# Kernel optimization log

Measured on AMD Instinct MI355X. Metric: run time of the kernel, lower is better.

## Reference

```python
import jax, jax.numpy as jnp
import numpy as np

HIDDEN = 2048
HEADS = 16
HEAD_DIM = HIDDEN // HEADS


def setup_inputs() -> dict:
    key = jax.random.key(0)
    ks = jax.random.split(key, 9)
    s = 0.02
    return {
        "hidden_state": jax.random.normal(ks[0], (2, 2048, HIDDEN), dtype=jnp.float32),
        "Wq": jax.random.normal(ks[1], (HIDDEN, HIDDEN), dtype=jnp.float32) * s,
        "bq": jnp.zeros((HIDDEN,), dtype=jnp.float32),
        "Wk": jax.random.normal(ks[2], (HIDDEN, HIDDEN), dtype=jnp.float32) * s,
        "bk": jnp.zeros((HIDDEN,), dtype=jnp.float32),
        "Wv": jax.random.normal(ks[3], (HIDDEN, HIDDEN), dtype=jnp.float32) * s,
        "bv": jnp.zeros((HIDDEN,), dtype=jnp.float32),
        "Wo": jax.random.normal(ks[4], (HIDDEN, HIDDEN), dtype=jnp.float32) * s,
        "bo": jnp.zeros((HIDDEN,), dtype=jnp.float32),
    }


def _split_head(x):
    b, s, _ = x.shape
    return x.reshape(b, s, HEADS, HEAD_DIM).transpose(0, 2, 1, 3)  # [B,H,S,D]


def reference(hidden_state, Wq, bq, Wk, bk, Wv, bv, Wo, bo):
    scale = 1.0 / (HEAD_DIM ** 0.5)
    # nn.Linear: x @ W.T + b
    q = _split_head(hidden_state @ Wq.T + bq)
    k = _split_head(hidden_state @ Wk.T + bk)
    v = _split_head(hidden_state @ Wv.T + bv)
    scores = jnp.einsum("bhqd,bhkd->bhqk", q, k) * scale  # [B,H,S,S]
    probs = jax.nn.softmax(scores, axis=-1)
    # dropout treated as identity (eval mode)
    out = jnp.einsum("bhqk,bhkd->bhqd", probs, v)  # [B,H,S,D]
    b, h, s, d = out.shape
    out = out.transpose(0, 2, 1, 3).reshape(b, s, h * d)
    return out @ Wo.T + bo
```

## Files before the change

kernel.cpp:

```cpp
#include <hip/hip_runtime.h>
#include <hip/hip_bf16.h>


typedef __attribute__((ext_vector_type(8))) short bf16x8;
typedef __attribute__((ext_vector_type(4))) float f32x4;
typedef unsigned short ushort_t;

#define MFMA_16x16x32(a, b, c) __builtin_amdgcn_mfma_f32_16x16x32_bf16((a), (b), (c), 0, 0, 0)

__device__ __forceinline__ ushort_t f2bf(float f) {
  unsigned int u = __builtin_bit_cast(unsigned int, f);
  u += 0x7fffu + ((u >> 16) & 1u);
  return (ushort_t)(u >> 16);
}

__device__ __forceinline__ void gload_lds16(const void* g, void* lds) {
  __builtin_amdgcn_global_load_lds(
      (const __attribute__((address_space(1))) unsigned int*)g,
      (__attribute__((address_space(3))) unsigned int*)(unsigned int)(unsigned long long)lds,
      16, 0, 0);
}

__global__ __launch_bounds__(256) void f2bf_kernel(const float* __restrict__ in,
                                                   ushort_t* __restrict__ out, int n4) {
  int i = blockIdx.x * blockDim.x + threadIdx.x;
  const int stride = gridDim.x * blockDim.x;
  for (; i < n4; i += stride) {
    const float4 v = ((const float4*)in)[i];
    ushort4 o;
    o.x = f2bf(v.x); o.y = f2bf(v.y); o.z = f2bf(v.z); o.w = f2bf(v.w);
    ((ushort4*)out)[i] = o;
  }
}

template <int SWAPV>
__global__ __launch_bounds__(512) void qkv_gemm(
    const ushort_t* __restrict__ A,
    const ushort_t* __restrict__ W,
    const float* __restrict__ bq, const float* __restrict__ bk,
    const float* __restrict__ bv,
    ushort_t* __restrict__ Qs, ushort_t* __restrict__ Ks,
    ushort_t* __restrict__ Vts, int nbx, int bcol0) {
  constexpr int K = 2048, NT = K / 32;
  extern __shared__ char sm[];
  const int tid = threadIdx.x;
  const int wave = tid >> 6, lane = tid & 63;
  const int g = lane >> 4, l15 = lane & 15;
  const int wr = wave >> 2, wc = wave & 3;

  const int bid = blockIdx.x;
  const int chunk = (nbx * 16) >> 3;
  const int sw = (bid & 7) * chunk + (bid >> 3);
  const int bx = sw % nbx, by = sw / nbx;
  const int brow = by * 256, bcol = bcol0 + bx * 256;

  const ushort_t* srcA[2];
  const ushort_t* srcB[2];
#pragma unroll
  for (int j = 0; j < 2; ++j) {
    const int p = (wave * 2 + j) * 64 + lane;
    const int row = p >> 2;
    const int col = (p & 3) ^ ((row >> 1) & 3);
    srcA[j] = A + (size_t)(brow + row) * K + col * 8;
    srcB[j] = W + (size_t)(bcol + row) * K + col * 8;
  }

  const int fph = (l15 >> 1) & 3;
  const int aOff = (wr * 128 + l15) * 64 + ((g ^ fph) << 4);
  const int bOff = (wc * 64 + l15) * 64 + ((g ^ fph) << 4) + 16384;

  char* p0 = sm;
  char* p1 = sm + 32768;
  char* p2 = sm + 65536;

#define STAGE_A(P, t)                                                        \
  {                                                                          \
    gload_lds16(srcA[0] + (t) * 32, (P) + (wave * 2 + 0) * 1024);            \
    gload_lds16(srcA[1] + (t) * 32, (P) + (wave * 2 + 1) * 1024);            \
  }
#define STAGE_B(P, t)                                                        \
  {                                                                          \
    gload_lds16(srcB[0] + (t) * 32, (P) + 16384 + (wave * 2 + 0) * 1024);    \
    gload_lds16(srcB[1] + (t) * 32, (P) + 16384 + (wave * 2 + 1) * 1024);    \
  }

  const f32x4 fzero = {0.f, 0.f, 0.f, 0.f};
  f32x4 acc[8][4];
#pragma unroll
  for (int i = 0; i < 8; ++i)
#pragma unroll
    for (int j = 0; j < 4; ++j) acc[i][j] = fzero;

  STAGE_A(p0, 0); STAGE_B(p0, 0);
  STAGE_A(p1, 1); STAGE_B(p1, 1);
  asm volatile("s_waitcnt vmcnt(4)" ::: "memory");
  __builtin_amdgcn_sched_barrier(0);
  __builtin_amdgcn_s_barrier();
  __builtin_amdgcn_sched_barrier(0);

  for (int kt = 0; kt < NT; ++kt) {
    const bool doStage = (kt < NT - 2);
    if (doStage) STAGE_A(p2, kt + 2);
    bf16x8 bfr[4], afr[4];
#pragma unroll
    for (int j = 0; j < 4; ++j) bfr[j] = *(const bf16x8*)(p0 + bOff + j * 1024);
#pragma unroll
    for (int i = 0; i < 4; ++i) afr[i] = *(const bf16x8*)(p0 + aOff + i * 1024);
    __builtin_amdgcn_s_setprio(1);
#pragma unroll
    for (int i = 0; i < 4; ++i)
#pragma unroll
      for (int j = 0; j < 4; ++j)
        acc[i][j] = SWAPV ? MFMA_16x16x32(bfr[j], afr[i], acc[i][j])
                          : MFMA_16x16x32(afr[i], bfr[j], acc[i][j]);
    __builtin_amdgcn_s_setprio(0);
    if (doStage) STAGE_B(p2, kt + 2);
#pragma unroll
    for (int i = 0; i < 4; ++i) afr[i] = *(const bf16x8*)(p0 + aOff + (4 + i) * 1024);
    __builtin_amdgcn_s_setprio(1);
#pragma unroll
    for (int i = 0; i < 4; ++i)
#pragma unroll
      for (int j = 0; j < 4; ++j)
        acc[4 + i][j] = SWAPV ? MFMA_16x16x32(bfr[j], afr[i], acc[4 + i][j])
                              : MFMA_16x16x32(afr[i], bfr[j], acc[4 + i][j]);
    __builtin_amdgcn_s_setprio(0);
    if (doStage) {
      asm volatile("s_waitcnt vmcnt(4) lgkmcnt(0)" ::: "memory");
    } else {
      asm volatile("s_waitcnt vmcnt(0) lgkmcnt(0)" ::: "memory");
    }
    __builtin_amdgcn_sched_barrier(0);
    __builtin_amdgcn_s_barrier();
    __builtin_amdgcn_sched_barrier(0);
    char* t = p0; p0 = p1; p1 = p2; p2 = t;
  }
#undef STAGE_A
#undef STAGE_B

  if (!SWAPV) {
    const int seg = bcol >> 11;
    const float* bias = (seg == 0) ? bq : bk;
    ushort_t* out = (seg == 0) ? Qs : Ks;
#pragma unroll
    for (int j = 0; j < 4; ++j) {
      const int n = (bcol + wc * 64 + j * 16 + l15) & 2047;
      const float bb = bias[n];
      const int h = n >> 7, d = n & 127;
#pragma unroll
      for (int i = 0; i < 8; ++i) {
#pragma unroll
        for (int r = 0; r < 4; ++r) {
          const int grow = brow + wr * 128 + i * 16 + g * 4 + r;
          const int b_ = grow >> 11, s_ = grow & 2047;
          out[(((size_t)b_ * 16 + h) * 2048 + s_) * 128 + d] =
              f2bf(acc[i][j][r] + bb);
        }
      }
    }
  } else {
#pragma unroll
    for (int j = 0; j < 4; ++j) {
#pragma unroll
      for (int r = 0; r < 4; ++r) {
        const int n = (bcol + wc * 64 + j * 16 + g * 4 + r) & 2047;
        const float bb = bv[n];
        const int h = n >> 7, d = n & 127;
#pragma unroll
        for (int i = 0; i < 8; ++i) {
          const int m = brow + wr * 128 + i * 16 + l15;
          const int b_ = m >> 11, s_ = m & 2047;
          Vts[(((size_t)b_ * 16 + h) * 128 + d) * 2048 + s_] =
              f2bf(acc[i][j][r] + bb);
        }
      }
    }
  }
}

__global__ __launch_bounds__(256) void gemm_bt_kernel(const ushort_t* __restrict__ A,
                                                      const ushort_t* __restrict__ B,
                                                      const float* __restrict__ bias,
                                                      float* __restrict__ Cout,
                                                      int M, int N, int K) {
  __shared__ __align__(16) char smem[16384];
  char* sA = smem;
  char* sB = smem + 8192;
  const int tid = threadIdx.x;
  const int wave = tid >> 6;
  const int lane = tid & 63;
  const int wr = wave >> 1, wc = wave & 1;
  const int brow = blockIdx.y * 128;
  const int bcol = blockIdx.x * 128;

  const f32x4 fzero = {0.f, 0.f, 0.f, 0.f};
  f32x4 acc[4][4];
#pragma unroll
  for (int i = 0; i < 4; ++i)
#pragma unroll
    for (int j = 0; j < 4; ++j) acc[i][j] = fzero;

  const int srow = lane >> 2;
  const int koff = (lane & 3) * 8;

  for (int kt = 0; kt < K; kt += 32) {
#pragma unroll
    for (int c = 0; c < 2; ++c) {
      const int ch = wave + c * 4;
      gload_lds16(A + (size_t)(brow + ch * 16 + srow) * K + kt + koff, sA + ch * 1024);
      gload_lds16(B + (size_t)(bcol + ch * 16 + srow) * K + kt + koff, sB + ch * 1024);
    }
    __syncthreads();
    bf16x8 af[4], bfr[4];
#pragma unroll
    for (int i = 0; i < 4; ++i)
      af[i] = *(const bf16x8*)(sA + (wr * 64 + i * 16 + (lane & 15)) * 64 + (lane >> 4) * 16);
#pragma unroll
    for (int j = 0; j < 4; ++j)
      bfr[j] = *(const bf16x8*)(sB + (wc * 64 + j * 16 + (lane & 15)) * 64 + (lane >> 4) * 16);
#pragma unroll
    for (int i = 0; i < 4; ++i)
#pragma unroll
      for (int j = 0; j < 4; ++j) acc[i][j] = MFMA_16x16x32(af[i], bfr[j], acc[i][j]);
    __syncthreads();
  }

#pragma unroll
  for (int i = 0; i < 4; ++i)
#pragma unroll
    for (int j = 0; j < 4; ++j)
#pragma unroll
      for (int r = 0; r < 4; ++r) {
        const int row = brow + wr * 64 + i * 16 + (lane >> 4) * 4 + r;
        const int col = bcol + wc * 64 + j * 16 + (lane & 15);
        Cout[(size_t)row * N + col] = acc[i][j][r] + bias[col];
      }
}

__global__ __launch_bounds__(256) void attn_kernel(const ushort_t* __restrict__ Q,
                                                   const ushort_t* __restrict__ K,
                                                   const ushort_t* __restrict__ Vt,
                                                   ushort_t* __restrict__ O) {
  constexpr int S = 2048, D = 128, H = 16;
  __shared__ __align__(16) char smem[16384 + 16384 + 9216];
  char* sK = smem;
  char* sVt = smem + 16384;
  char* sP = smem + 32768;

  const int tid = threadIdx.x;
  const int wave = tid >> 6;
  const int lane = tid & 63;
  const int g = lane >> 4;
  const int l15 = lane & 15;
  const int qt = blockIdx.x & 31;
  const int bh = blockIdx.x >> 5;
  const int b = bh >> 4, h = bh & 15;

  const ushort_t* Qb = Q + (size_t)bh * S * D;
  const char* Kb = (const char*)(K + (size_t)bh * S * D);
  const char* Vtb = (const char*)(Vt + (size_t)bh * D * S);
  const int q0 = qt * 64 + wave * 16;

  bf16x8 aq[4];
  {
    const ushort_t* qrow = Qb + (size_t)(q0 + l15) * D + g * 8;
#pragma unroll
    for (int kk = 0; kk < 4; ++kk) aq[kk] = *(const bf16x8*)(qrow + kk * 32);
  }

  const char* kg[4];
  const char* vg[4];
#pragma unroll
  for (int i = 0; i < 4; ++i) {
    const int po = (wave * 4 + i) * 1024 + lane * 16;
    const int lk = po ^ (((po >> 8) & 7) << 4);
    kg[i] = Kb + (size_t)(lk >> 8) * 256 + (lk & 255);
    const int lv = po ^ (((po >> 7) & 7) << 4);
    vg[i] = Vtb + (size_t)(lv >> 7) * 4096 + (lv & 127);
  }

  const f32x4 fzero = {0.f, 0.f, 0.f, 0.f};
  f32x4 o[8];
#pragma unroll
  for (int nt = 0; nt < 8; ++nt) o[nt] = fzero;
  float row_m[4] = {-1e30f, -1e30f, -1e30f, -1e30f};
  float row_l[4] = {0.f, 0.f, 0.f, 0.f};

  bf16x8 ones;
#pragma unroll
  for (int i = 0; i < 8; ++i) ones[i] = (short)0x3F80;

  char* sPw = sP + wave * 2304;
  const float SC = 0.12751746f;
  const float THR = 90.0f;

  for (int kv0 = 0; kv0 < S; kv0 += 64) {
    __syncthreads();
#pragma unroll
    for (int i = 0; i < 4; ++i)
      gload_lds16(kg[i] + (size_t)kv0 * 256, sK + (wave * 4 + i) * 1024);
#pragma unroll
    for (int i = 0; i < 4; ++i)
      gload_lds16(vg[i] + (size_t)kv0 * 2, sVt + (wave * 4 + i) * 1024);
    __syncthreads();

    f32x4 sfrag[4];
#pragma unroll
    for (int nt = 0; nt < 4; ++nt) {
      sfrag[nt] = fzero;
#pragma unroll
      for (int kk = 0; kk < 4; ++kk) {
        const int row = nt * 16 + l15;
        const int la = row * 256 + kk * 64 + g * 16;
        const bf16x8 bk = *(const bf16x8*)(sK + (la ^ ((row & 7) << 4)));
        sfrag[nt] = MFMA_16x16x32(aq[kk], bk, sfrag[nt]);
      }
    }

#pragma unroll
    for (int r = 0; r < 4; ++r) {
      const float s0 = sfrag[0][r];
      const float s1 = sfrag[1][r];
      const float s2 = sfrag[2][r];
      const float s3 = sfrag[3][r];
      const float lm = fmaxf(fmaxf(s0, s1), fmaxf(s2, s3));
      if (!__all(lm - row_m[r] <= THR)) {
        float mx = lm;
        mx = fmaxf(mx, __shfl_xor(mx, 1));
        mx = fmaxf(mx, __shfl_xor(mx, 2));
        mx = fmaxf(mx, __shfl_xor(mx, 4));
        mx = fmaxf(mx, __shfl_xor(mx, 8));
        const float nm = fmaxf(row_m[r], mx);
        const float corr = exp2f((row_m[r] - nm) * SC);
        row_l[r] *= corr;
#pragma unroll
        for (int nt = 0; nt < 8; ++nt) o[nt][r] *= corr;
        row_m[r] = nm;
      }
      const float nm = row_m[r];
      const float p0 = exp2f((s0 - nm) * SC);
      const float p1 = exp2f((s1 - nm) * SC);
      const float p2 = exp2f((s2 - nm) * SC);
      const float p3 = exp2f((s3 - nm) * SC);
      unsigned int pk01, pk23;
      asm("v_cvt_pk_bf16_f32 %0, %1, %2" : "=v"(pk01) : "v"(p0), "v"(p1));
      asm("v_cvt_pk_bf16_f32 %0, %1, %2" : "=v"(pk23) : "v"(p2), "v"(p3));
      ushort_t* pr = (ushort_t*)(sPw + (g * 4 + r) * 144);
      pr[l15] = (ushort_t)(pk01 & 0xffffu);
      pr[16 + l15] = (ushort_t)(pk01 >> 16);
      pr[32 + l15] = (ushort_t)(pk23 & 0xffffu);
      pr[48 + l15] = (ushort_t)(pk23 >> 16);
    }

    const bf16x8 pa0 = *(const bf16x8*)(sPw + l15 * 144 + g * 16);
    const bf16x8 pa1 = *(const bf16x8*)(sPw + l15 * 144 + 64 + g * 16);
    f32x4 lfrag = fzero;
    lfrag = MFMA_16x16x32(pa0, ones, lfrag);
    lfrag = MFMA_16x16x32(pa1, ones, lfrag);
#pragma unroll
    for (int nt = 0; nt < 8; ++nt) {
      const int d = nt * 16 + l15;
      const int la0 = d * 128 + g * 16;
      const bf16x8 bv0 = *(const bf16x8*)(sVt + (la0 ^ ((d & 7) << 4)));
      o[nt] = MFMA_16x16x32(pa0, bv0, o[nt]);
      const bf16x8 bv1 = *(const bf16x8*)(sVt + ((la0 + 64) ^ ((d & 7) << 4)));
      o[nt] = MFMA_16x16x32(pa1, bv1, o[nt]);
    }
#pragma unroll
    for (int r = 0; r < 4; ++r) row_l[r] += lfrag[r];
  }

#pragma unroll
  for (int r = 0; r < 4; ++r) {
    const float inv = 1.0f / row_l[r];
    const int srow = q0 + g * 4 + r;
    ushort_t* orow = O + ((size_t)b * S + srow) * (H * D) + h * D;
#pragma unroll
    for (int nt = 0; nt < 8; ++nt) orow[nt * 16 + l15] = f2bf(o[nt][r] * inv);
  }
}

extern "C" void kernel_launch(void* const* d_in, const int* in_sizes, int n_in,
                              void* d_out, int out_size, void* d_ws, size_t ws_size,
                              hipStream_t stream) {
  const float* hidden = (const float*)d_in[0];
  const float* Wq = (const float*)d_in[1];
  const float* bq = (const float*)d_in[2];
  const float* Wk = (const float*)d_in[3];
  const float* bk = (const float*)d_in[4];
  const float* Wv = (const float*)d_in[5];
  const float* bv = (const float*)d_in[6];
  const float* Wo = (const float*)d_in[7];
  const float* bo = (const float*)d_in[8];

  constexpr int M = 4096, N = 2048, Kd = 2048;
  char* ws = (char*)d_ws;
  ushort_t* hb   = (ushort_t*)(ws);
  ushort_t* wqkv = (ushort_t*)(ws + (16u << 20));
  ushort_t* wob  = (ushort_t*)(ws + (40u << 20));
  ushort_t* Qs   = (ushort_t*)(ws + (48u << 20));
  ushort_t* Ks   = Qs + (size_t)M * N;
  ushort_t* Vts  = Ks + (size_t)M * N;
  ushort_t* AO   = Vts + (size_t)M * N;

  f2bf_kernel<<<2048, 256, 0, stream>>>(hidden, hb, M * Kd / 4);
  f2bf_kernel<<<1024, 256, 0, stream>>>(Wq, wqkv, N * Kd / 4);
  f2bf_kernel<<<1024, 256, 0, stream>>>(Wk, wqkv + (size_t)N * Kd, N * Kd / 4);
  f2bf_kernel<<<1024, 256, 0, stream>>>(Wv, wqkv + 2 * (size_t)N * Kd, N * Kd / 4);
  f2bf_kernel<<<1024, 256, 0, stream>>>(Wo, wob, N * Kd / 4);

  qkv_gemm<0><<<256, 512, 98304, stream>>>(hb, wqkv, bq, bk, bv, Qs, Ks, Vts, 16, 0);
  qkv_gemm<1><<<128, 512, 98304, stream>>>(hb, wqkv, bq, bk, bv, Qs, Ks, Vts, 8, 4096);
  attn_kernel<<<1024, 256, 0, stream>>>(Qs, Ks, Vts, AO);
  dim3 gg(N / 128, M / 128);
  gemm_bt_kernel<<<gg, 256, 0, stream>>>(AO, wob, bo, (float*)d_out, M, N, Kd);
}
```

Baseline: 489.5 us.

## Replace output projection with triple-buffered 256x256 tiled GEMM and merge weight casts

Replaces the simple 128x128 output-projection GEMM with a 512-thread kernel using 256x256 tiles. It triple-buffers LDS loads with swizzled layout, interleaves staging with MFMA, and raises wave priority during MFMA. The four weight bf16 conversion launches are merged into one kernel, and attention is split into two launches over halves of the batch-heads. The larger tiles launch only 128 blocks, which may underfill the GPU.

```diff
diff --git a/kernel.cpp b/kernel.cpp
--- a/kernel.cpp
+++ b/kernel.cpp
@@ -26,6 +26,24 @@
   int i = blockIdx.x * blockDim.x + threadIdx.x;
   const int stride = gridDim.x * blockDim.x;
   for (; i < n4; i += stride) {
+    const float4 v = ((const float4*)in)[i];
+    ushort4 o;
+    o.x = f2bf(v.x); o.y = f2bf(v.y); o.z = f2bf(v.z); o.w = f2bf(v.w);
+    ((ushort4*)out)[i] = o;
+  }
+}
+
+__global__ __launch_bounds__(256) void f2bfw_kernel(
+    const float* __restrict__ w0, const float* __restrict__ w1,
+    const float* __restrict__ w2, const float* __restrict__ w3,
+    ushort_t* __restrict__ o0, ushort_t* __restrict__ o1,
+    ushort_t* __restrict__ o2, ushort_t* __restrict__ o3) {
+  const int seg = blockIdx.x >> 9;
+  const int bid = blockIdx.x & 511;
+  const float* in = (seg == 0) ? w0 : (seg == 1) ? w1 : (seg == 2) ? w2 : w3;
+  ushort_t* out = (seg == 0) ? o0 : (seg == 1) ? o1 : (seg == 2) ? o2 : o3;
+  constexpr int n4 = 2048 * 2048 / 4;
+  for (int i = bid * 256 + (int)threadIdx.x; i < n4; i += 512 * 256) {
     const float4 v = ((const float4*)in)[i];
     ushort4 o;
     o.x = f2bf(v.x); o.y = f2bf(v.y); o.z = f2bf(v.z); o.w = f2bf(v.w);
@@ -178,69 +196,122 @@
   }
 }
 
-__global__ __launch_bounds__(256) void gemm_bt_kernel(const ushort_t* __restrict__ A,
-                                                      const ushort_t* __restrict__ B,
-                                                      const float* __restrict__ bias,
-                                                      float* __restrict__ Cout,
-                                                      int M, int N, int K) {
-  __shared__ __align__(16) char smem[16384];
-  char* sA = smem;
-  char* sB = smem + 8192;
+__global__ __launch_bounds__(512) void oproj_gemm(
+    const ushort_t* __restrict__ A,
+    const ushort_t* __restrict__ W,
+    const float* __restrict__ bias, float* __restrict__ Cout) {
+  constexpr int K = 2048, NT = K / 32, nbx = 8;
+  extern __shared__ char sm[];
   const int tid = threadIdx.x;
-  const int wave = tid >> 6;
-  const int lane = tid & 63;
-  const int wr = wave >> 1, wc = wave & 1;
-  const int brow = blockIdx.y * 128;
-  const int bcol = blockIdx.x * 128;
+  const int wave = tid >> 6, lane = tid & 63;
+  const int g = lane >> 4, l15 = lane & 15;
+  const int wr = wave >> 2, wc = wave & 3;
+
+  const int bid = blockIdx.x;
+  const int chunk = (nbx * 16) >> 3;
+  const int sw = (bid & 7) * chunk + (bid >> 3);
+  const int bx = sw % nbx, by = sw / nbx;
+  const int brow = by * 256, bcol = bx * 256;
+
+  const ushort_t* srcA[2];
+  const ushort_t* srcB[2];
+#pragma unroll
+  for (int j = 0; j < 2; ++j) {
+    const int p = (wave * 2 + j) * 64 + lane;
+    const int row = p >> 2;
+    const int col = (p & 3) ^ ((row >> 1) & 3);
+    srcA[j] = A + (size_t)(brow + row) * K + col * 8;
+    srcB[j] = W + (size_t)(bcol + row) * K + col * 8;
+  }
+
+  const int fph = (l15 >> 1) & 3;
+  const int aOff = (wr * 128 + l15) * 64 + ((g ^ fph) << 4);
+  const int bOff = (wc * 64 + l15) * 64 + ((g ^ fph) << 4) + 16384;
+
+  char* p0 = sm;
+  char* p1 = sm + 32768;
+  char* p2 = sm + 65536;
+
+#define STAGE_A(P, t)                                                        \
+  {                                                                          \
+    gload_lds16(srcA[0] + (t) * 32, (P) + (wave * 2 + 0) * 1024);            \
+    gload_lds16(srcA[1] + (t) * 32, (P) + (wave * 2 + 1) * 1024);            \
+  }
+#define STAGE_B(P, t)                                                        \
+  {                                                                          \
+    gload_lds16(srcB[0] + (t) * 32, (P) + 16384 + (wave * 2 + 0) * 1024);    \
+    gload_lds16(srcB[1] + (t) * 32, (P) + 16384 + (wave * 2 + 1) * 1024);    \
+  }
 
   const f32x4 fzero = {0.f, 0.f, 0.f, 0.f};
-  f32x4 acc[4][4];
-#pragma unroll
-  for (int i = 0; i < 4; ++i)
+  f32x4 acc[8][4];
+#pragma unroll
+  for (int i = 0; i < 8; ++i)
 #pragma unroll
     for (int j = 0; j < 4; ++j) acc[i][j] = fzero;
 
-  const int srow = lane >> 2;
-  const int koff = (lane & 3) * 8;
-
-  for (int kt = 0; kt < K; kt += 32) {
-#pragma unroll
-    for (int c = 0; c < 2; ++c) {
-      const int ch = wave + c * 4;
-      gload_lds16(A + (size_t)(brow + ch * 16 + srow) * K + kt + koff, sA + ch * 1024);
-      gload_lds16(B + (size_t)(bcol + ch * 16 + srow) * K + kt + koff, sB + ch * 1024);
-    }
-    __syncthreads();
-    bf16x8 af[4], bfr[4];
-#pragma unroll
-    for (int i = 0; i < 4; ++i)
-      af[i] = *(const bf16x8*)(sA + (wr * 64 + i * 16 + (lane & 15)) * 64 + (lane >> 4) * 16);
-#pragma unroll
-    for (int j = 0; j < 4; ++j)
-      bfr[j] = *(const bf16x8*)(sB + (wc * 64 + j * 16 + (lane & 15)) * 64 + (lane >> 4) * 16);
-#pragma unroll
-    for (int i = 0; i < 4; ++i)
-#pragma unroll
-      for (int j = 0; j < 4; ++j) acc[i][j] = MFMA_16x16x32(af[i], bfr[j], acc[i][j]);
-    __syncthreads();
-  }
-
-#pragma unroll
-  for (int i = 0; i < 4; ++i)
-#pragma unroll
-    for (int j = 0; j < 4; ++j)
+  STAGE_A(p0, 0); STAGE_B(p0, 0);
+  STAGE_A(p1, 1); STAGE_B(p1, 1);
+  asm volatile("s_waitcnt vmcnt(4)" ::: "memory");
+  __builtin_amdgcn_sched_barrier(0);
+  __builtin_amdgcn_s_barrier();
+  __builtin_amdgcn_sched_barrier(0);
+
+  for (int kt = 0; kt < NT; ++kt) {
+    const bool doStage = (kt < NT - 2);
+    if (doStage) STAGE_A(p2, kt + 2);
+    bf16x8 bfr[4], afr[4];
+#pragma unroll
+    for (int j = 0; j < 4; ++j) bfr[j] = *(const bf16x8*)(p0 + bOff + j * 1024);
+#pragma unroll
+    for (int i = 0; i < 4; ++i) afr[i] = *(const bf16x8*)(p0 + aOff + i * 1024);
+    __builtin_amdgcn_s_setprio(1);
+#pragma unroll
+    for (int i = 0; i < 4; ++i)
+#pragma unroll
+      for (int j = 0; j < 4; ++j) acc[i][j] = MFMA_16x16x32(afr[i], bfr[j], acc[i][j]);
+    __builtin_amdgcn_s_setprio(0);
+    if (doStage) STAGE_B(p2, kt + 2);
+#pragma unroll
+    for (int i = 0; i < 4; ++i) afr[i] = *(const bf16x8*)(p0 + aOff + (4 + i) * 1024);
+    __builtin_amdgcn_s_setprio(1);
+#pragma unroll
+    for (int i = 0; i < 4; ++i)
+#pragma unroll
+      for (int j = 0; j < 4; ++j) acc[4 + i][j] = MFMA_16x16x32(afr[i], bfr[j], acc[4 + i][j]);
+    __builtin_amdgcn_s_setprio(0);
+    if (doStage) {
+      asm volatile("s_waitcnt vmcnt(4) lgkmcnt(0)" ::: "memory");
+    } else {
+      asm volatile("s_waitcnt vmcnt(0) lgkmcnt(0)" ::: "memory");
+    }
+    __builtin_amdgcn_sched_barrier(0);
+    __builtin_amdgcn_s_barrier();
+    __builtin_amdgcn_sched_barrier(0);
+    char* t = p0; p0 = p1; p1 = p2; p2 = t;
+  }
+#undef STAGE_A
+#undef STAGE_B
+
+#pragma unroll
+  for (int j = 0; j < 4; ++j) {
+    const int col = bcol + wc * 64 + j * 16 + l15;
+    const float bb = bias[col];
+#pragma unroll
+    for (int i = 0; i < 8; ++i) {
 #pragma unroll
       for (int r = 0; r < 4; ++r) {
-        const int row = brow + wr * 64 + i * 16 + (lane >> 4) * 4 + r;
-        const int col = bcol + wc * 64 + j * 16 + (lane & 15);
-        Cout[(size_t)row * N + col] = acc[i][j][r] + bias[col];
+        const int row = brow + wr * 128 + i * 16 + g * 4 + r;
+        Cout[(size_t)row * 2048 + col] = acc[i][j][r] + bb;
       }
+    }
+  }
 }
 
 __global__ __launch_bounds__(256) void attn_kernel(const ushort_t* __restrict__ Q,
                                                    const ushort_t* __restrict__ K,
                                                    const ushort_t* __restrict__ Vt,
-                                                   ushort_t* __restrict__ O) {
+                                                   ushort_t* __restrict__ O, int bh0) {
   constexpr int S = 2048, D = 128, H = 16;
   __shared__ __align__(16) char smem[16384 + 16384 + 9216];
   char* sK = smem;
@@ -253,7 +324,7 @@
   const int g = lane >> 4;
   const int l15 = lane & 15;
   const int qt = blockIdx.x & 31;
-  const int bh = blockIdx.x >> 5;
+  const int bh = bh0 + (blockIdx.x >> 5);
   const int b = bh >> 4, h = bh & 15;
 
   const ushort_t* Qb = Q + (size_t)bh * S * D;
@@ -404,14 +475,13 @@
   ushort_t* AO   = Vts + (size_t)M * N;
 
   f2bf_kernel<<<2048, 256, 0, stream>>>(hidden, hb, M * Kd / 4);
-  f2bf_kernel<<<1024, 256, 0, stream>>>(Wq, wqkv, N * Kd / 4);
-  f2bf_kernel<<<1024, 256, 0, stream>>>(Wk, wqkv + (size_t)N * Kd, N * Kd / 4);
-  f2bf_kernel<<<1024, 256, 0, stream>>>(Wv, wqkv + 2 * (size_t)N * Kd, N * Kd / 4);
-  f2bf_kernel<<<1024, 256, 0, stream>>>(Wo, wob, N * Kd / 4);
+  f2bfw_kernel<<<2048, 256, 0, stream>>>(Wq, Wk, Wv, Wo, wqkv,
+                                         wqkv + (size_t)N * Kd,
+                                         wqkv + 2 * (size_t)N * Kd, wob);
 
   qkv_gemm<0><<<256, 512, 98304, stream>>>(hb, wqkv, bq, bk, bv, Qs, Ks, Vts, 16, 0);
   qkv_gemm<1><<<128, 512, 98304, stream>>>(hb, wqkv, bq, bk, bv, Qs, Ks, Vts, 8, 4096);
-  attn_kernel<<<1024, 256, 0, stream>>>(Qs, Ks, Vts, AO);
-  dim3 gg(N / 128, M / 128);
-  gemm_bt_kernel<<<gg, 256, 0, stream>>>(AO, wob, bo, (float*)d_out, M, N, Kd);
-}
+  attn_kernel<<<512, 256, 0, stream>>>(Qs, Ks, Vts, AO, 0);
+  attn_kernel<<<512, 256, 0, stream>>>(Qs, Ks, Vts, AO, 16);
+  oproj_gemm<<<128, 512, 98304, stream>>>(AO, wob, bo, (float*)d_out);
+}
```

Result: no change. 485.4 us (-0.8%).
